# Kernel optimization log

Measured on AMD Instinct MI355X. Metric: run time of the kernel, lower is better.

## Reference

```python
import jax, jax.numpy as jnp
import numpy as np

N = 4096      # total_activities_num
D = 128       # feature dim
E = 1_000_000 # number of edges (events)
EPS = 1e-12


def setup_inputs() -> dict:
    key = jax.random.key(0)
    k1, k2, k3, k4, k5 = jax.random.split(key, 5)
    currents = jax.random.randint(k1, (E,), 0, N, dtype=jnp.int64)
    targets = jax.random.randint(k2, (E,), 0, N, dtype=jnp.int64)
    activities_features = jax.random.normal(k3, (N, D), dtype=jnp.float32)
    cases_features = jax.random.normal(k4, (E, D), dtype=jnp.float32)
    # Learned parameter W [N, N], kaiming_uniform fan_in relu -> U(-b, b), b = sqrt(6/fan_in)
    bound = float(np.sqrt(6.0 / N))
    W = jax.random.uniform(k5, (N, N), dtype=jnp.float32, minval=-bound, maxval=bound)
    return {
        "currents": currents,
        "targets": targets,
        "activities_features": activities_features,
        "cases_features": cases_features,
        "W": W,
    }


def reference(currents, targets, activities_features, cases_features, W):
    # Per-edge gather: h_emb, t_emb are [E, D]
    h_emb = activities_features[currents]
    t_emb = activities_features[targets]
    # dist = ||h + case - t||_2 per edge -> [E]
    diff = h_emb + cases_features - t_emb
    dist = jnp.sqrt(jnp.sum(diff * diff, axis=1))
    vals = jnp.exp(-dist)
    # Scatter-add into dense [N, N] attention input at (tail, head)
    att_input = jnp.zeros((N, N), dtype=activities_features.dtype)
    att_input = att_input.at[targets, currents].add(vals)
    # Row-normalize
    norm = jnp.sum(att_input, axis=1, keepdims=True)
    attention = att_input / (norm + EPS)
    # Dense GEMMs
    feat = W @ activities_features           # [N, D]
    h = attention @ feat + feat               # [N, D]
    return h
```

## Files before the change

### kernel.cpp

```cpp
#include <hip/hip_runtime.h>
#include <hip/hip_bf16.h>

typedef unsigned short u16;
typedef unsigned int   u32;

typedef __attribute__((ext_vector_type(8))) __bf16 bf16x8;
typedef __attribute__((ext_vector_type(4))) float  f32x4;

#define NN 4096
#define DD 128
#define EPS 1e-12f

#define KS 4
#define BM 32
#define BK 128
#define KPER (NN / KS)
#define LDK 136

static __device__ __forceinline__ u16 f2bf(float f) {
    union { float f; u32 u; } v; v.f = f;
    u32 r = v.u + 0x7fffu + ((v.u >> 16) & 1u);
    return (u16)(r >> 16);
}

__global__ __launch_bounds__(256) void edge_kernel(
    const int* __restrict__ currents, const int* __restrict__ targets,
    const float* __restrict__ A, const float* __restrict__ cases,
    float* __restrict__ att, int E)
{
    int e = blockIdx.x * 8 + (threadIdx.x >> 5);
    if (e >= E) return;
    int l = threadIdx.x & 31;
    int c = currents[e];
    int t = targets[e];
    float4 h = *(const float4*)(A + (size_t)c * DD + l * 4);
    float4 g = *(const float4*)(A + (size_t)t * DD + l * 4);
    float4 q = *(const float4*)(cases + (size_t)e * DD + l * 4);
    float d0 = h.x + q.x - g.x;
    float d1 = h.y + q.y - g.y;
    float d2 = h.z + q.z - g.z;
    float d3 = h.w + q.w - g.w;
    float s = d0 * d0 + d1 * d1 + d2 * d2 + d3 * d3;
#pragma unroll
    for (int m = 16; m; m >>= 1) s += __shfl_xor(s, m, 64);
    if (l == 0) {
        float val = __expf(-__fsqrt_rn(s));
        atomicAdd(att + (size_t)t * NN + c, val);
    }
}

__global__ __launch_bounds__(256) void transpose_to_bf16(
    const float* __restrict__ in, u16* __restrict__ out)
{
    __shared__ __align__(16) u16 lds[128][40];
    const int k0 = blockIdx.x * 32;
    const int t = threadIdx.x;
#pragma unroll
    for (int i = 0; i < 4; ++i) {
        int f  = t + 256 * i;
        int kr = f >> 5;
        int n0 = (f & 31) * 4;
        float4 v = *(const float4*)(in + (size_t)(k0 + kr) * DD + n0);
        lds[n0 + 0][kr] = f2bf(v.x);
        lds[n0 + 1][kr] = f2bf(v.y);
        lds[n0 + 2][kr] = f2bf(v.z);
        lds[n0 + 3][kr] = f2bf(v.w);
    }
    __syncthreads();
    int n = t >> 1, h = t & 1;
    uint4 v0 = *(const uint4*)&lds[n][h * 16];
    uint4 v1 = *(const uint4*)&lds[n][h * 16 + 8];
    *(uint4*)(out + (size_t)n * NN + k0 + h * 16)     = v0;
    *(uint4*)(out + (size_t)n * NN + k0 + h * 16 + 8) = v1;
}

template<bool ROWSUM>
__global__ __launch_bounds__(512, 4) void gemm_splitk(
    const float* __restrict__ Amat,
    const u16*   __restrict__ BT,
    float* __restrict__ part,
    float* __restrict__ normsum)
{
    __shared__ __align__(16) u16 As[BM * LDK];
    __shared__ __align__(16) u16 Bs[DD * LDK];

    const int m0   = blockIdx.x * BM;
    const int ks   = blockIdx.y;
    const int kbeg = ks * KPER;
    const int t    = threadIdx.x;
    const int wave = t >> 6;
    const int lane = t & 63;
    const int quad = lane >> 4;
    const int l16  = lane & 15;

    const int ar = t >> 4;
    const int aq = t & 15;
    const int bn = t >> 2;
    const int bq = t & 3;

    const float* Ap = Amat + (size_t)(m0 + ar) * NN + kbeg + aq * 4;
    const u16*   Bp = BT   + (size_t)bn * NN + kbeg + bq * 32;

    float4 va0 = *(const float4*)(Ap);
    float4 va1 = *(const float4*)(Ap + 64);
    uint4  vb0 = *(const uint4*)(Bp);
    uint4  vb1 = *(const uint4*)(Bp + 8);
    uint4  vb2 = *(const uint4*)(Bp + 16);
    uint4  vb3 = *(const uint4*)(Bp + 24);

    f32x4 acc0 = {0.f, 0.f, 0.f, 0.f};
    f32x4 acc1 = {0.f, 0.f, 0.f, 0.f};
    float rsum = 0.f;

    for (int kk = 0; kk < KPER; kk += BK) {
        if (ROWSUM) {
            rsum += (va0.x + va0.y) + (va0.z + va0.w)
                  + (va1.x + va1.y) + (va1.z + va1.w);
        }
        ushort4 u0, u1;
        u0.x = f2bf(va0.x); u0.y = f2bf(va0.y); u0.z = f2bf(va0.z); u0.w = f2bf(va0.w);
        u1.x = f2bf(va1.x); u1.y = f2bf(va1.y); u1.z = f2bf(va1.z); u1.w = f2bf(va1.w);
        *(ushort4*)&As[ar * LDK + aq * 4]      = u0;
        *(ushort4*)&As[ar * LDK + aq * 4 + 64] = u1;
        *(uint4*)&Bs[bn * LDK + bq * 32]      = vb0;
        *(uint4*)&Bs[bn * LDK + bq * 32 + 8]  = vb1;
        *(uint4*)&Bs[bn * LDK + bq * 32 + 16] = vb2;
        *(uint4*)&Bs[bn * LDK + bq * 32 + 24] = vb3;
        __syncthreads();

        if (kk + BK < KPER) {
            int k1 = kk + BK;
            va0 = *(const float4*)(Ap + k1);
            va1 = *(const float4*)(Ap + k1 + 64);
            vb0 = *(const uint4*)(Bp + k1);
            vb1 = *(const uint4*)(Bp + k1 + 8);
            vb2 = *(const uint4*)(Bp + k1 + 16);
            vb3 = *(const uint4*)(Bp + k1 + 24);
        }

#pragma unroll
        for (int k2 = 0; k2 < 4; ++k2) {
            bf16x8 a0 = *(const bf16x8*)&As[l16 * LDK + k2 * 32 + quad * 8];
            bf16x8 a1 = *(const bf16x8*)&As[(16 + l16) * LDK + k2 * 32 + quad * 8];
            bf16x8 b  = *(const bf16x8*)&Bs[(wave * 16 + l16) * LDK + k2 * 32 + quad * 8];
            acc0 = __builtin_amdgcn_mfma_f32_16x16x32_bf16(a0, b, acc0, 0, 0, 0);
            acc1 = __builtin_amdgcn_mfma_f32_16x16x32_bf16(a1, b, acc1, 0, 0, 0);
        }
        __syncthreads();
    }

    float* P = part + (size_t)ks * NN * DD;
#pragma unroll
    for (int r = 0; r < 4; ++r) {
        int row0 = m0 + quad * 4 + r;
        int col  = wave * 16 + l16;
        P[(size_t)row0 * DD + col]        = acc0[r];
        P[(size_t)(row0 + 16) * DD + col] = acc1[r];
    }

    if (ROWSUM) {
#pragma unroll
        for (int m = 8; m; m >>= 1) rsum += __shfl_xor(rsum, m, 64);
        if ((t & 15) == 0) atomicAdd(normsum + m0 + ar, rsum);
    }
}

__global__ __launch_bounds__(256) void combine_feat(
    const float* __restrict__ part, float* __restrict__ feat)
{
    int i = blockIdx.x * 256 + threadIdx.x;
    const float4* p = (const float4*)part;
    const int S = NN * DD / 4;
    float4 a = p[i], b = p[i + S], c = p[i + 2 * S], d = p[i + 3 * S];
    float4 s;
    s.x = (a.x + b.x) + (c.x + d.x);
    s.y = (a.y + b.y) + (c.y + d.y);
    s.z = (a.z + b.z) + (c.z + d.z);
    s.w = (a.w + b.w) + (c.w + d.w);
    ((float4*)feat)[i] = s;
}

__global__ __launch_bounds__(256) void combine_out(
    const float* __restrict__ part, const float* __restrict__ normsum,
    const float* __restrict__ feat, float* __restrict__ out)
{
    int i = blockIdx.x * 256 + threadIdx.x;
    int row = i >> 5;
    const float4* p = (const float4*)part;
    const int S = NN * DD / 4;
    float4 a = p[i], b = p[i + S], c = p[i + 2 * S], d = p[i + 3 * S];
    float sc = 1.0f / (normsum[row] + EPS);
    float4 f = ((const float4*)feat)[i];
    float4 s;
    s.x = ((a.x + b.x) + (c.x + d.x)) * sc + f.x;
    s.y = ((a.y + b.y) + (c.y + d.y)) * sc + f.y;
    s.z = ((a.z + b.z) + (c.z + d.z)) * sc + f.z;
    s.w = ((a.w + b.w) + (c.w + d.w)) * sc + f.w;
    ((float4*)out)[i] = s;
}

extern "C" void kernel_launch(void* const* d_in, const int* in_sizes, int n_in,
                              void* d_out, int out_size, void* d_ws, size_t ws_size,
                              hipStream_t stream)
{
    const int*   currents = (const int*)d_in[0];
    const int*   targets  = (const int*)d_in[1];
    const float* acts     = (const float*)d_in[2];
    const float* cases    = (const float*)d_in[3];
    const float* W        = (const float*)d_in[4];
    float*       out      = (float*)d_out;
    const int E = in_sizes[0];

    char* ws = (char*)d_ws;
    float* att     = (float*)ws;
    float* part    = (float*)(ws + (size_t)NN * NN * 4);
    float* feat    = part + (size_t)KS * NN * DD;
    u16*   BT1     = (u16*)(feat + (size_t)NN * DD);
    u16*   BT2     = BT1 + (size_t)DD * NN;
    float* normsum = (float*)(BT2 + (size_t)DD * NN);

    hipMemsetAsync(att, 0, (size_t)NN * NN * 4, stream);
    hipMemsetAsync(normsum, 0, (size_t)NN * 4, stream);

    transpose_to_bf16<<<128, 256, 0, stream>>>(acts, BT1);

    edge_kernel<<<(E + 7) / 8, 256, 0, stream>>>(currents, targets, acts, cases,
                                                 att, E);

    gemm_splitk<false><<<dim3(NN / BM, KS), 512, 0, stream>>>(W, BT1, part, nullptr);
    combine_feat<<<NN * DD / 4 / 256, 256, 0, stream>>>(part, feat);

    transpose_to_bf16<<<128, 256, 0, stream>>>(feat, BT2);

    gemm_splitk<true><<<dim3(NN / BM, KS), 512, 0, stream>>>(att, BT2, part, normsum);
    combine_out<<<NN * DD / 4 / 256, 256, 0, stream>>>(part, normsum, feat, out);
}
```

Before: 214.9 us.

## Store scatter attention matrix in bf16 with packed atomics and feed GEMM directly

The dense N×N attention accumulator becomes bf16 instead of fp32. The edge kernel scatter-adds through packed bf16x2 atomics, with a CAS fallback when no hardware atomic is available. The second GEMM then reads bf16 A tiles directly without conversion. This halves memset and GEMM read traffic on the largest buffer, at the cost of bf16 accumulation error in the scatter sums. Nontemporal loads are also added for the streamed case features and the GEMM A operand.

```diff
diff --git a/kernel.cpp b/kernel.cpp
--- a/kernel.cpp
+++ b/kernel.cpp
@@ -6,6 +6,7 @@
 
 typedef __attribute__((ext_vector_type(8))) __bf16 bf16x8;
 typedef __attribute__((ext_vector_type(4))) float  f32x4;
+typedef __attribute__((ext_vector_type(4))) u32    u32x4;
 
 #define NN 4096
 #define DD 128
@@ -22,20 +23,44 @@
     u32 r = v.u + 0x7fffu + ((v.u >> 16) & 1u);
     return (u16)(r >> 16);
 }
+static __device__ __forceinline__ float bf2f(u16 u) {
+    union { u32 i; float f; } v; v.i = (u32)u << 16; return v.f;
+}
+
+template <typename T>
+static __device__ __forceinline__ auto bf2_atomic_add(T* p, T v, int)
+    -> decltype(unsafeAtomicAdd(p, v), void()) {
+    unsafeAtomicAdd(p, v);
+}
+template <typename T>
+static __device__ __forceinline__ void bf2_atomic_add(T* p, T v, long) {
+    u32* w = (u32*)p;
+    union { u32 i; T h; } av; av.h = v;
+    float alo = bf2f((u16)(av.i & 0xffff));
+    float ahi = bf2f((u16)(av.i >> 16));
+    u32 old = *w, assumed;
+    do {
+        assumed = old;
+        float lo = bf2f((u16)(assumed & 0xffff)) + alo;
+        float hi = bf2f((u16)(assumed >> 16)) + ahi;
+        u32 nv = (u32)f2bf(lo) | ((u32)f2bf(hi) << 16);
+        old = atomicCAS(w, assumed, nv);
+    } while (old != assumed);
+}
 
 __global__ __launch_bounds__(256) void edge_kernel(
     const int* __restrict__ currents, const int* __restrict__ targets,
     const float* __restrict__ A, const float* __restrict__ cases,
-    float* __restrict__ att, int E)
+    u16* __restrict__ att, int E)
 {
     int e = blockIdx.x * 8 + (threadIdx.x >> 5);
     if (e >= E) return;
     int l = threadIdx.x & 31;
     int c = currents[e];
     int t = targets[e];
-    float4 h = *(const float4*)(A + (size_t)c * DD + l * 4);
-    float4 g = *(const float4*)(A + (size_t)t * DD + l * 4);
-    float4 q = *(const float4*)(cases + (size_t)e * DD + l * 4);
+    f32x4 h = *(const f32x4*)(A + (size_t)c * DD + l * 4);
+    f32x4 g = *(const f32x4*)(A + (size_t)t * DD + l * 4);
+    f32x4 q = __builtin_nontemporal_load((const f32x4*)(cases + (size_t)e * DD + l * 4));
     float d0 = h.x + q.x - g.x;
     float d1 = h.y + q.y - g.y;
     float d2 = h.z + q.z - g.z;
@@ -45,7 +70,11 @@
     for (int m = 16; m; m >>= 1) s += __shfl_xor(s, m, 64);
     if (l == 0) {
         float val = __expf(-__fsqrt_rn(s));
-        atomicAdd(att + (size_t)t * NN + c, val);
+        u16 b = f2bf(val);
+        size_t off = (size_t)t * NN + c;
+        union { u32 i; __hip_bfloat162 h2; } pk;
+        pk.i = (c & 1) ? ((u32)b << 16) : (u32)b;
+        bf2_atomic_add((__hip_bfloat162*)(att + (off & ~(size_t)1)), pk.h2, 0);
     }
 }
 
@@ -74,10 +103,10 @@
     *(uint4*)(out + (size_t)n * NN + k0 + h * 16 + 8) = v1;
 }
 
-template<bool ROWSUM>
+template<bool ROWSUM, bool ABF16>
 __global__ __launch_bounds__(512, 4) void gemm_splitk(
-    const float* __restrict__ Amat,
-    const u16*   __restrict__ BT,
+    const void* __restrict__ AmatV,
+    const u16*  __restrict__ BT,
     float* __restrict__ part,
     float* __restrict__ normsum)
 {
@@ -98,30 +127,47 @@
     const int bn = t >> 2;
     const int bq = t & 3;
 
-    const float* Ap = Amat + (size_t)(m0 + ar) * NN + kbeg + aq * 4;
-    const u16*   Bp = BT   + (size_t)bn * NN + kbeg + bq * 32;
-
-    float4 va0 = *(const float4*)(Ap);
-    float4 va1 = *(const float4*)(Ap + 64);
-    uint4  vb0 = *(const uint4*)(Bp);
-    uint4  vb1 = *(const uint4*)(Bp + 8);
-    uint4  vb2 = *(const uint4*)(Bp + 16);
-    uint4  vb3 = *(const uint4*)(Bp + 24);
+    const float* Apf = (const float*)AmatV + (size_t)(m0 + ar) * NN + kbeg + aq * 4;
+    const u16*   Aph = (const u16*)AmatV   + (size_t)(m0 + ar) * NN + kbeg + aq * 8;
+    const u16*   Bp  = BT + (size_t)bn * NN + kbeg + bq * 32;
+
+    f32x4 va0, va1; u32x4 vah;
+    if constexpr (ABF16) {
+        vah = __builtin_nontemporal_load((const u32x4*)Aph);
+    } else {
+        va0 = __builtin_nontemporal_load((const f32x4*)Apf);
+        va1 = __builtin_nontemporal_load((const f32x4*)(Apf + 64));
+    }
+    uint4 vb0 = *(const uint4*)(Bp);
+    uint4 vb1 = *(const uint4*)(Bp + 8);
+    uint4 vb2 = *(const uint4*)(Bp + 16);
+    uint4 vb3 = *(const uint4*)(Bp + 24);
 
     f32x4 acc0 = {0.f, 0.f, 0.f, 0.f};
     f32x4 acc1 = {0.f, 0.f, 0.f, 0.f};
     float rsum = 0.f;
 
     for (int kk = 0; kk < KPER; kk += BK) {
-        if (ROWSUM) {
-            rsum += (va0.x + va0.y) + (va0.z + va0.w)
-                  + (va1.x + va1.y) + (va1.z + va1.w);
+        if constexpr (ABF16) {
+            if (ROWSUM) {
+#pragma unroll
+            for (int j = 0; j < 4; ++j) {
+                u32 w = vah[j];
+                rsum += bf2f((u16)(w & 0xffff)) + bf2f((u16)(w >> 16));
+            }
+            }
+            *(u32x4*)&As[ar * LDK + aq * 8] = vah;
+        } else {
+            if (ROWSUM) {
+                rsum += (va0.x + va0.y) + (va0.z + va0.w)
+                      + (va1.x + va1.y) + (va1.z + va1.w);
+            }
+            ushort4 u0, u1;
+            u0.x = f2bf(va0.x); u0.y = f2bf(va0.y); u0.z = f2bf(va0.z); u0.w = f2bf(va0.w);
+            u1.x = f2bf(va1.x); u1.y = f2bf(va1.y); u1.z = f2bf(va1.z); u1.w = f2bf(va1.w);
+            *(ushort4*)&As[ar * LDK + aq * 4]      = u0;
+            *(ushort4*)&As[ar * LDK + aq * 4 + 64] = u1;
         }
-        ushort4 u0, u1;
-        u0.x = f2bf(va0.x); u0.y = f2bf(va0.y); u0.z = f2bf(va0.z); u0.w = f2bf(va0.w);
-        u1.x = f2bf(va1.x); u1.y = f2bf(va1.y); u1.z = f2bf(va1.z); u1.w = f2bf(va1.w);
-        *(ushort4*)&As[ar * LDK + aq * 4]      = u0;
-        *(ushort4*)&As[ar * LDK + aq * 4 + 64] = u1;
         *(uint4*)&Bs[bn * LDK + bq * 32]      = vb0;
         *(uint4*)&Bs[bn * LDK + bq * 32 + 8]  = vb1;
         *(uint4*)&Bs[bn * LDK + bq * 32 + 16] = vb2;
@@ -130,8 +176,12 @@
 
         if (kk + BK < KPER) {
             int k1 = kk + BK;
-            va0 = *(const float4*)(Ap + k1);
-            va1 = *(const float4*)(Ap + k1 + 64);
+            if constexpr (ABF16) {
+                vah = __builtin_nontemporal_load((const u32x4*)(Aph + k1));
+            } else {
+                va0 = __builtin_nontemporal_load((const f32x4*)(Apf + k1));
+                va1 = __builtin_nontemporal_load((const f32x4*)(Apf + k1 + 64));
+            }
             vb0 = *(const uint4*)(Bp + k1);
             vb1 = *(const uint4*)(Bp + k1 + 8);
             vb2 = *(const uint4*)(Bp + k1 + 16);
@@ -212,14 +262,14 @@
     const int E = in_sizes[0];
 
     char* ws = (char*)d_ws;
-    float* att     = (float*)ws;
-    float* part    = (float*)(ws + (size_t)NN * NN * 4);
+    u16*   att     = (u16*)ws;
+    float* part    = (float*)(ws + (size_t)NN * NN * 2);
     float* feat    = part + (size_t)KS * NN * DD;
     u16*   BT1     = (u16*)(feat + (size_t)NN * DD);
     u16*   BT2     = BT1 + (size_t)DD * NN;
     float* normsum = (float*)(BT2 + (size_t)DD * NN);
 
-    hipMemsetAsync(att, 0, (size_t)NN * NN * 4, stream);
+    hipMemsetAsync(att, 0, (size_t)NN * NN * 2, stream);
     hipMemsetAsync(normsum, 0, (size_t)NN * 4, stream);
 
     transpose_to_bf16<<<128, 256, 0, stream>>>(acts, BT1);
@@ -227,11 +277,11 @@
     edge_kernel<<<(E + 7) / 8, 256, 0, stream>>>(currents, targets, acts, cases,
                                                  att, E);
 
-    gemm_splitk<false><<<dim3(NN / BM, KS), 512, 0, stream>>>(W, BT1, part, nullptr);
+    gemm_splitk<false, false><<<dim3(NN / BM, KS), 512, 0, stream>>>(W, BT1, part, nullptr);
     combine_feat<<<NN * DD / 4 / 256, 256, 0, stream>>>(part, feat);
 
     transpose_to_bf16<<<128, 256, 0, stream>>>(feat, BT2);
 
-    gemm_splitk<true><<<dim3(NN / BM, KS), 512, 0, stream>>>(att, BT2, part, normsum);
+    gemm_splitk<true, true><<<dim3(NN / BM, KS), 512, 0, stream>>>(att, BT2, part, normsum);
     combine_out<<<NN * DD / 4 / 256, 256, 0, stream>>>(part, normsum, feat, out);
 }
```

New measurement: 197.5 us. 1.09x faster.
